# Kernel optimization log

Hardware: AMD Instinct MI355X
Metric: run time of the kernel (lower is better)

The kernel has to match this reference:

```python
import jax, jax.numpy as jnp
import numpy as np

Cl, Nl, Cv, Nv, M = 32, 128, 8, 64, 500000


def _sample1d(line, g):
    # line: [C, N]; g in [-1,1]; align_corners=True, zeros padding
    C, N = line.shape
    ix = (g + 1.0) * 0.5 * (N - 1)
    i0 = jnp.floor(ix)
    w = ix - i0
    i0 = i0.astype(jnp.int32)
    def gth(i, wt):
        valid = (i >= 0) & (i < N)
        return line[:, jnp.clip(i, 0, N - 1)] * (wt * valid)
    return (gth(i0, 1.0 - w) + gth(i0 + 1, w)).T  # [M, C]


def _sample2d(plane, gx, gy):
    # plane: [C, H, W]; grid x -> W axis, y -> H axis (torch grid_sample convention)
    C, H, W = plane.shape
    ix = (gx + 1.0) * 0.5 * (W - 1)
    iy = (gy + 1.0) * 0.5 * (H - 1)
    x0 = jnp.floor(ix); y0 = jnp.floor(iy)
    wx = ix - x0; wy = iy - y0
    x0 = x0.astype(jnp.int32); y0 = y0.astype(jnp.int32)
    flat = plane.reshape(C, -1)
    def gth(xi, yi, wt):
        valid = (xi >= 0) & (xi < W) & (yi >= 0) & (yi < H)
        idx = jnp.clip(yi, 0, H - 1) * W + jnp.clip(xi, 0, W - 1)
        return flat[:, idx] * (wt * valid)
    out = (gth(x0, y0, (1 - wx) * (1 - wy)) + gth(x0 + 1, y0, wx * (1 - wy))
           + gth(x0, y0 + 1, (1 - wx) * wy) + gth(x0 + 1, y0 + 1, wx * wy))
    return out.T  # [M, C]


def _sample3d(vol, gx, gy, gz):
    # vol: [C, D, H, W]; grid (x,y,z) -> (W,H,D) axes
    C, D, H, W = vol.shape
    ix = (gx + 1.0) * 0.5 * (W - 1)
    iy = (gy + 1.0) * 0.5 * (H - 1)
    iz = (gz + 1.0) * 0.5 * (D - 1)
    x0 = jnp.floor(ix); y0 = jnp.floor(iy); z0 = jnp.floor(iz)
    wx = ix - x0; wy = iy - y0; wz = iz - z0
    x0 = x0.astype(jnp.int32); y0 = y0.astype(jnp.int32); z0 = z0.astype(jnp.int32)
    flat = vol.reshape(C, -1)
    out = 0.0
    for dz in (0, 1):
        for dy in (0, 1):
            for dx in (0, 1):
                xi, yi, zi = x0 + dx, y0 + dy, z0 + dz
                wt = ((wx if dx else 1 - wx) * (wy if dy else 1 - wy) * (wz if dz else 1 - wz))
                valid = (xi >= 0) & (xi < W) & (yi >= 0) & (yi < H) & (zi >= 0) & (zi < D)
                idx = (jnp.clip(zi, 0, D - 1) * H + jnp.clip(yi, 0, H - 1)) * W + jnp.clip(xi, 0, W - 1)
                out = out + flat[:, idx] * (wt * valid)
    return out.T  # [M, C]


def setup_inputs() -> dict:
    key = jax.random.key(0)
    ks = jax.random.split(key, 16)
    rng, shift = 0.4, 0.1
    coordinates = jax.random.uniform(ks[0], (1, M, 3), minval=-1.0, maxval=1.0)
    line_x = jax.random.uniform(ks[1], (Cl, Nl)) * rng + shift
    line_y = jax.random.uniform(ks[2], (Cl, Nl)) * rng + shift
    line_z = jax.random.uniform(ks[3], (Cl, Nl)) * rng + shift
    plane_xy = jax.random.normal(ks[4], (Cl, Nl, Nl)) * rng + shift
    plane_yz = jax.random.normal(ks[5], (Cl, Nl, Nl)) * rng + shift
    plane_xz = jax.random.normal(ks[6], (Cl, Nl, Nl)) * rng + shift
    volume = jax.random.normal(ks[7], (Cv, Nv, Nv, Nv)) * rng + shift
    def lin(k, fi, fo):
        k1, k2 = jax.random.split(k)
        lim = 1.0 / np.sqrt(fi)
        return (jax.random.uniform(k1, (fi, fo), minval=-lim, maxval=lim),
                jax.random.uniform(k2, (fo,), minval=-lim, maxval=lim))
    Wx, bx = lin(ks[8], Cl, Cl)
    Wy, by = lin(ks[9], Cl, Cl)
    Wz, bz = lin(ks[10], Cl, Cl)
    W1, b1 = lin(ks[11], Cl + Cv, 128)
    W2, b2 = lin(ks[12], 128, 1)
    return dict(coordinates=coordinates, line_x=line_x, line_y=line_y, line_z=line_z,
                plane_xy=plane_xy, plane_yz=plane_yz, plane_xz=plane_xz, volume=volume,
                Wx=Wx, bx=bx, Wy=Wy, by=by, Wz=Wz, bz=bz, W1=W1, b1=b1, W2=W2, b2=b2)


def reference(coordinates, line_x, line_y, line_z, plane_xy, plane_yz, plane_xz, volume,
              Wx, bx, Wy, by, Wz, bz, W1, b1, W2, b2):
    c = coordinates[0]  # [M, 3], batch squeezed like the torch code
    x, y, z = c[:, 0], c[:, 1], c[:, 2]
    x_e = _sample1d(line_x, x)
    y_e = _sample1d(line_y, y)
    z_e = _sample1d(line_z, z)
    xy_e = _sample2d(plane_xy, x, y)
    yz_e = _sample2d(plane_yz, y, z)
    xz_e = _sample2d(plane_xz, x, z)
    xyz_e = _sample3d(volume, x, y, z)
    phi = lambda e, W, b: jax.nn.relu(e) @ W + b  # Sequential(ReLU, Linear)
    yztran = phi(yz_e, Wx, bx)
    xztran = phi(xz_e, Wy, by)
    xytran = phi(xy_e, Wz, bz)
    xtran = phi(x_e, Wx, bx)
    ytran = phi(y_e, Wy, by)
    ztran = phi(z_e, Wz, bz)
    features = xtran * yztran + ytran * xztran + ztran * xytran
    features = jnp.concatenate([features, xyz_e], axis=-1)  # [M, Cl+Cv]
    h = jax.nn.relu(features @ W1 + b1)
    return h @ W2 + b2  # [M, 1]
```

## Files before the change

### kernel.cpp

```cpp
#include <hip/hip_runtime.h>

typedef unsigned short u16;
typedef u16 u16x8 __attribute__((ext_vector_type(8)));
typedef _Float16 half2 __attribute__((ext_vector_type(2)));
typedef _Float16 h8v __attribute__((ext_vector_type(8)));
typedef float f4v __attribute__((ext_vector_type(4)));

union H8 { h8v v; half2 p[4]; };

static __device__ __forceinline__ float bf2f(u16 u) {
    union { unsigned int i; float f; } v;
    v.i = ((unsigned int)u) << 16;
    return v.f;
}
static __device__ __forceinline__ u16 f2bf(float f) {
    union { float f; unsigned int i; } v;
    v.f = f;
    unsigned int x = v.i;
    x += 0x7fffu + ((x >> 16) & 1u);
    return (u16)(x >> 16);
}
static __device__ __forceinline__ float gld(int dt, const void* p, int i) {
    return dt ? ((const float*)p)[i] : bf2f(((const u16*)p)[i]);
}
static __device__ __forceinline__ int detect_dt(const void* coords) {
    u16 v = ((const u16*)coords)[threadIdx.x & 63];
    int e = (v >> 7) & 0xFF;
    bool inr = (e >= 90) && (e <= 126);
    unsigned long long m = __ballot(inr);
    return (__popcll(m) >= 56) ? 0 : 1;
}
static __device__ __forceinline__ half2 pk(float a, float b) {
    return __builtin_bit_cast(half2, __builtin_amdgcn_cvt_pkrtz(a, b));
}

static __device__ __forceinline__ void lds_wait() {
    asm volatile("s_waitcnt lgkmcnt(0)" ::: "memory");
}

#define WF_OFF        64u
#define PLANES_S_OFF  34304u
#define VOL_S_OFF     3180032u
#define LINES_S_OFF   7374336u
#define PART_OFF      7398912u
#define TOT_OFF       9496064u
#define ORDER_OFF     9512448u

#define NBUCK 4096
#define HBLOCKS 256

static __device__ __forceinline__ int make_key3(float x, float y, float z) {
    int kx = min(max((int)((x + 1.0f) * 8.0f), 0), 15);
    int ky = min(max((int)((y + 1.0f) * 8.0f), 0), 15);
    int kz = min(max((int)((z + 1.0f) * 8.0f), 0), 15);
    return (kz * 16 + ky) * 16 + kx;
}
static __device__ __forceinline__ int make_key(int dt, const void* coords, int p) {
    return make_key3(gld(dt, coords, p * 3 + 0), gld(dt, coords, p * 3 + 1),
                     gld(dt, coords, p * 3 + 2));
}

static __device__ __forceinline__ void weights_work(
    int dt, int r,
    const void* Wx, const void* bx, const void* Wy, const void* by,
    const void* Wz, const void* bz, const void* W1, const void* b1,
    const void* W2, const void* b2, float* wbase)
{
    _Float16* WtH = (_Float16*)wbase;
    float*    bv  = wbase + 1536;
    _Float16* W1H = (_Float16*)(wbase + 1632);
    float*    b1v = wbase + 5728;
    float*    W2v = wbase + 5856;
    float*    b2v = wbase + 5984;
    if (r < 3072) {
        int m = r >> 10, idx = r & 1023;
        int o = idx >> 5, c = idx & 31;
        const void* s = (m == 0) ? Wx : (m == 1) ? Wy : Wz;
        WtH[r] = (_Float16)gld(dt, s, c * 32 + o);
    } else if (r < 3168) {
        int q2 = r - 3072;
        int m = q2 >> 5, c = q2 & 31;
        const void* s = (m == 0) ? bx : (m == 1) ? by : bz;
        bv[q2] = gld(dt, s, c);
    } else if (r < 11360) {
        int idx = r - 3168;
        int j = idx >> 6, i = idx & 63;
        W1H[idx] = (i < 40) ? (_Float16)gld(dt, W1, i * 128 + j) : (_Float16)0.0f;
    } else if (r < 11488) {
        b1v[r - 11360] = gld(dt, b1, r - 11360);
    } else if (r < 11616) {
        W2v[r - 11488] = gld(dt, W2, r - 11488);
    } else if (r == 11616) {
        b2v[0] = gld(dt, b2, 0);
    }
}

__global__ __launch_bounds__(256) void kp_prep_all(
    const void* __restrict__ coords,
    const void* __restrict__ lx, const void* __restrict__ ly,
    const void* __restrict__ lz,
    const void* __restrict__ pxy, const void* __restrict__ pyz,
    const void* __restrict__ pxz, const void* __restrict__ vol,
    const void* __restrict__ Wx, const void* __restrict__ bx,
    const void* __restrict__ Wy, const void* __restrict__ by,
    const void* __restrict__ Wz, const void* __restrict__ bz,
    const void* __restrict__ W1, const void* __restrict__ b1,
    const void* __restrict__ W2, const void* __restrict__ b2,
    float* __restrict__ wbase,
    u16* __restrict__ planes_s, u16* __restrict__ vol_s,
    u16* __restrict__ lines_s, u16* __restrict__ part, int M)
{
    __shared__ unsigned int lh[NBUCK];
    int dt = detect_dt(coords);
    int blk = blockIdx.x;
    if (blk < 1798) {
        int t = blk * 256 + threadIdx.x;
        u16x8 v;
        if (t < 196608) {
            int o = t * 8;
            int pl = o >> 19;
            int r  = o & 524287;
            int pos = r >> 5, c0 = r & 31;
            const void* src = (pl == 0) ? pxy : (pl == 1) ? pyz : pxz;
#pragma unroll
            for (int i = 0; i < 8; ++i)
                v[i] = dt ? f2bf(((const float*)src)[(c0 + i) * 16384 + pos])
                          : ((const u16*)src)[(c0 + i) * 16384 + pos];
            *(u16x8*)(planes_s + o) = v;
        } else if (t < 458752) {
            int pos = t - 196608;
#pragma unroll
            for (int c = 0; c < 8; ++c)
                v[c] = dt ? f2bf(((const float*)vol)[c * 262144 + pos])
                          : ((const u16*)vol)[c * 262144 + pos];
            *(u16x8*)(vol_s + pos * 8) = v;
        } else {
            int o = (t - 458752) * 8;
            int l = o >> 12, rr = o & 4095;
            int pos = rr >> 5, c0 = rr & 31;
            const void* src = (l == 0) ? lx : (l == 1) ? ly : lz;
#pragma unroll
            for (int i = 0; i < 8; ++i)
                v[i] = dt ? f2bf(((const float*)src)[(c0 + i) * 128 + pos])
                          : ((const u16*)src)[(c0 + i) * 128 + pos];
            *(u16x8*)(lines_s + o) = v;
        }
    } else if (blk < 1844) {
        int r = (blk - 1798) * 256 + threadIdx.x;
        weights_work(dt, r, Wx, bx, Wy, by, Wz, bz, W1, b1, W2, b2, wbase);
    } else {
        int b = blk - 1844;
        for (int i = threadIdx.x; i < NBUCK; i += 256) lh[i] = 0u;
        __syncthreads();
        for (int p = b * 256 + threadIdx.x; p < M; p += HBLOCKS * 256)
            atomicAdd(&lh[make_key(dt, coords, p)], 1u);
        __syncthreads();
        for (int i = threadIdx.x; i < NBUCK; i += 256)
            part[b * NBUCK + i] = (u16)lh[i];
    }
}

__global__ __launch_bounds__(256) void kp_colscan(
    u16* __restrict__ part, unsigned int* __restrict__ tot)
{
    int lane = threadIdx.x & 63;
    int bkt  = blockIdx.x * 4 + (threadIdx.x >> 6);
    unsigned int v[4];
    unsigned int ltot = 0;
#pragma unroll
    for (int i = 0; i < 4; ++i) {
        v[i] = part[(lane * 4 + i) * NBUCK + bkt];
        ltot += v[i];
    }
    unsigned int x = ltot;
#pragma unroll
    for (int d = 1; d < 64; d <<= 1) {
        unsigned int y = __shfl_up(x, d);
        if (lane >= d) x += y;
    }
    unsigned int run = x - ltot;
#pragma unroll
    for (int i = 0; i < 4; ++i) {
        part[(lane * 4 + i) * NBUCK + bkt] = (u16)run;
        run += v[i];
    }
    if (lane == 63) tot[bkt] = x;
}

__global__ __launch_bounds__(256) void kp_scatter_det(
    const void* __restrict__ coords, const u16* __restrict__ part,
    const unsigned int* __restrict__ tot,
    int* __restrict__ order, u16* __restrict__ scoords, int M)
{
    __shared__ unsigned int cnt[NBUCK];
    __shared__ unsigned int psum[256];
    int b = blockIdx.x;
    int t = threadIdx.x;
    unsigned int bs[16];
    unsigned int s = 0;
#pragma unroll
    for (int i = 0; i < 16; ++i) {
        bs[i] = tot[t * 16 + i];
        s += bs[i];
    }
    psum[t] = s;
    __syncthreads();
#pragma unroll
    for (int d = 1; d < 256; d <<= 1) {
        unsigned int v = (t >= d) ? psum[t - d] : 0u;
        __syncthreads();
        psum[t] += v;
        __syncthreads();
    }
    unsigned int run = psum[t] - s;
#pragma unroll
    for (int i = 0; i < 16; ++i) {
        int bkt = t * 16 + i;
        cnt[bkt] = run + (unsigned int)part[b * NBUCK + bkt];
        run += bs[i];
    }
    __syncthreads();
    int dt = detect_dt(coords);
    const u16* cu = (const u16*)coords;
    for (int p = b * 256 + t; p < M; p += HBLOCKS * 256) {
        float x = gld(dt, coords, p * 3 + 0);
        float y = gld(dt, coords, p * 3 + 1);
        float z = gld(dt, coords, p * 3 + 2);
        int key = make_key3(x, y, z);
        unsigned int pos = atomicAdd(&cnt[key], 1u);
        order[pos] = p;
        if (dt == 0) {
            scoords[pos * 3 + 0] = cu[p * 3 + 0];
            scoords[pos * 3 + 1] = cu[p * 3 + 1];
            scoords[pos * 3 + 2] = cu[p * 3 + 2];
        }
    }
}

struct Samp { int i0, i1; float w0, w1; };

static __device__ __forceinline__ Samp make_samp(float g, int N) {
    float ix = (g + 1.0f) * 0.5f * (float)(N - 1);
    float fl = floorf(ix);
    float w  = ix - fl;
    int i  = (int)fl;
    int i1 = i + 1;
    float v0 = (i  >= 0 && i  < N) ? 1.0f : 0.0f;
    float v1 = (i1 >= 0 && i1 < N) ? 1.0f : 0.0f;
    Samp s;
    s.w0 = (1.0f - w) * v0;
    s.w1 = w * v1;
    s.i0 = min(max(i, 0), N - 1);
    s.i1 = min(max(i1, 0), N - 1);
    return s;
}

#define MFMA16(a, b, c) __builtin_amdgcn_mfma_f32_16x16x32_f16((a), (b), (c), 0, 0, 0)

#define SRE 34
#define SR2 68

struct PL { u16x8 q00[4], q01[4], q10[4], q11[4]; };
struct VL { u16x8 v[8]; };

static __device__ __forceinline__ void plane_load(
    const u16* __restrict__ Ps, const Samp& sa, const Samp& sb, PL& P)
{
    const u16x8* p00 = (const u16x8*)(Ps + (sb.i0 * 128 + sa.i0) * 32);
    const u16x8* p01 = (const u16x8*)(Ps + (sb.i0 * 128 + sa.i1) * 32);
    const u16x8* p10 = (const u16x8*)(Ps + (sb.i1 * 128 + sa.i0) * 32);
    const u16x8* p11 = (const u16x8*)(Ps + (sb.i1 * 128 + sa.i1) * 32);
#pragma unroll
    for (int cc = 0; cc < 4; ++cc) {
        P.q00[cc] = p00[cc]; P.q01[cc] = p01[cc];
        P.q10[cc] = p10[cc]; P.q11[cc] = p11[cc];
    }
}

static __device__ __forceinline__ void vol_loads(
    const u16* __restrict__ vol_s, const Samp& vx, const Samp& vy,
    const Samp& vz, VL& V)
{
#pragma unroll
    for (int corner = 0; corner < 8; ++corner) {
        int dx = corner & 1, dy = (corner >> 1) & 1, dz = corner >> 2;
        int xi = dx ? vx.i1 : vx.i0;
        int yi = dy ? vy.i1 : vy.i0;
        int zi = dz ? vz.i1 : vz.i0;
        V.v[corner] = *(const u16x8*)(vol_s + (((zi * 64) + yi) * 64 + xi) * 8);
    }
}

template<int PRE>
static __device__ __forceinline__ void term_step(
    int lane, int q, int l15,
    const u16* __restrict__ Ls, const Samp& sl,
    const PL& P, const Samp& sa, const Samp& sb,
    const _Float16* __restrict__ Wt, const float* __restrict__ bvt,
    _Float16* El, _Float16* Ep, float (&feat)[4][2][4],
    const u16* __restrict__ nps, const Samp& na, const Samp& nb, PL& PN,
    const u16* __restrict__ vol_s, const Samp& vx, const Samp& vy,
    const Samp& vz, VL& V)
{
    const u16x8* l0 = (const u16x8*)(Ls + sl.i0 * 32);
    const u16x8* l1 = (const u16x8*)(Ls + sl.i1 * 32);
    float w00 = sb.w0 * sa.w0, w01 = sb.w0 * sa.w1;
    float w10 = sb.w1 * sa.w0, w11 = sb.w1 * sa.w1;
#pragma unroll
    for (int cc = 0; cc < 4; ++cc) {
        u16x8 A0 = l0[cc], A1 = l1[cc];
        u16x8 Q00 = P.q00[cc], Q01 = P.q01[cc];
        u16x8 Q10 = P.q10[cc], Q11 = P.q11[cc];
        H8 hl, hp;
#pragma unroll
        for (int kk = 0; kk < 4; ++kk) {
            int k0 = 2 * kk, k1 = k0 + 1;
            float el0 = sl.w0 * bf2f(A0[k0]) + sl.w1 * bf2f(A1[k0]);
            float el1 = sl.w0 * bf2f(A0[k1]) + sl.w1 * bf2f(A1[k1]);
            float ep0 = w00 * bf2f(Q00[k0]) + w01 * bf2f(Q01[k0])
                      + w10 * bf2f(Q10[k0]) + w11 * bf2f(Q11[k0]);
            float ep1 = w00 * bf2f(Q00[k1]) + w01 * bf2f(Q01[k1])
                      + w10 * bf2f(Q10[k1]) + w11 * bf2f(Q11[k1]);
            hl.p[kk] = pk(fmaxf(el0, 0.0f), fmaxf(el1, 0.0f));
            hp.p[kk] = pk(fmaxf(ep0, 0.0f), fmaxf(ep1, 0.0f));
        }
        *(h8v*)&El[lane * SRE + cc * 8] = hl.v;
        *(h8v*)&Ep[lane * SRE + cc * 8] = hp.v;
    }
    if constexpr (PRE == 1) plane_load(nps, na, nb, PN);
    if constexpr (PRE == 2) vol_loads(vol_s, vx, vy, vz, V);

    h8v bf0 = *(const h8v*)&Wt[(l15) * 32 + q * 8];
    h8v bf1 = *(const h8v*)&Wt[(16 + l15) * 32 + q * 8];
    float bb0 = bvt[l15], bb1 = bvt[16 + l15];
    f4v c0 = {bb0, bb0, bb0, bb0};
    f4v c1 = {bb1, bb1, bb1, bb1};
    lds_wait();
#pragma unroll
    for (int mt = 0; mt < 4; ++mt) {
        h8v aL = *(const h8v*)&El[(mt * 16 + l15) * SRE + q * 8];
        h8v aP = *(const h8v*)&Ep[(mt * 16 + l15) * SRE + q * 8];
        f4v ta0 = MFMA16(aL, bf0, c0);
        f4v tb0 = MFMA16(aP, bf0, c0);
        f4v ta1 = MFMA16(aL, bf1, c1);
        f4v tb1 = MFMA16(aP, bf1, c1);
#pragma unroll
        for (int r = 0; r < 4; ++r) {
            feat[mt][0][r] += ta0[r] * tb0[r];
            feat[mt][1][r] += ta1[r] * tb1[r];
        }
    }
    lds_wait();
}

__global__ __launch_bounds__(64) void kp_main_mfma(
    const void* __restrict__ coords, const int* __restrict__ order,
    const u16* __restrict__ scoords,
    const u16* __restrict__ planes_s, const u16* __restrict__ vol_s,
    const u16* __restrict__ lines_s,
    const float* __restrict__ wbase,
    void* __restrict__ out, int M)
{
    __shared__ _Float16 eb[2 * 64 * SRE];
    __shared__ float res[64];
    int dt = detect_dt(coords);
    const _Float16* WtH = (const _Float16*)wbase;
    const float*    bv  = wbase + 1536;
    const _Float16* W1H = (const _Float16*)(wbase + 1632);
    const float*    b1v = wbase + 5728;
    const float*    W2v = wbase + 5856;
    const float*    b2v = wbase + 5984;

    int lane = threadIdx.x;
    int q = lane >> 4, l15 = lane & 15;
    _Float16* El = eb;
    _Float16* Ep = eb + 64 * SRE;
    _Float16* E2 = eb;

    int p = blockIdx.x * 64 + lane;
    p = min(p, M - 1);
    int sp = order[p];

    float x, y, z;
    if (dt == 0) {
        x = bf2f(scoords[p * 3 + 0]);
        y = bf2f(scoords[p * 3 + 1]);
        z = bf2f(scoords[p * 3 + 2]);
    } else {
        x = ((const float*)coords)[sp * 3 + 0];
        y = ((const float*)coords)[sp * 3 + 1];
        z = ((const float*)coords)[sp * 3 + 2];
    }

    Samp sx = make_samp(x, 128), sy = make_samp(y, 128), sz = make_samp(z, 128);

    float feat[4][2][4];
#pragma unroll
    for (int mt = 0; mt < 4; ++mt)
#pragma unroll
        for (int n = 0; n < 2; ++n)
#pragma unroll
            for (int r = 0; r < 4; ++r) feat[mt][n][r] = 0.0f;

    PL Pa, Pb;
    VL V;
    Samp vx, vy, vz;

    plane_load(planes_s + 1 * 524288, sy, sz, Pa);

    term_step<1>(lane, q, l15, lines_s + 0 * 4096, sx, Pa, sy, sz,
                 WtH + 0, bv + 0, El, Ep, feat,
                 planes_s + 2 * 524288, sx, sz, Pb,
                 vol_s, sx, sx, sx, V);

    term_step<1>(lane, q, l15, lines_s + 1 * 4096, sy, Pb, sx, sz,
                 WtH + 1024, bv + 32, El, Ep, feat,
                 planes_s + 0 * 524288, sx, sy, Pa,
                 vol_s, sx, sx, sx, V);

    vx = make_samp(x, 64); vy = make_samp(y, 64); vz = make_samp(z, 64);

    term_step<2>(lane, q, l15, lines_s + 2 * 4096, sz, Pa, sx, sy,
                 WtH + 2048, bv + 64, El, Ep, feat,
                 planes_s, sx, sy, Pb,
                 vol_s, vx, vy, vz, V);

#pragma unroll
    for (int mt = 0; mt < 4; ++mt)
#pragma unroll
        for (int n = 0; n < 2; ++n)
#pragma unroll
            for (int r = 0; r < 4; ++r)
                E2[(mt * 16 + q * 4 + r) * SR2 + n * 16 + l15] =
                    (_Float16)feat[mt][n][r];
    {
        float vf[8];
#pragma unroll
        for (int c = 0; c < 8; ++c) vf[c] = 0.0f;
#pragma unroll
        for (int corner = 0; corner < 8; ++corner) {
            int dx = corner & 1, dy = (corner >> 1) & 1, dz = corner >> 2;
            float w = (dx ? vx.w1 : vx.w0) * (dy ? vy.w1 : vy.w0)
                    * (dz ? vz.w1 : vz.w0);
            u16x8 v = V.v[corner];
#pragma unroll
            for (int c = 0; c < 8; ++c)
                vf[c] = fmaf(w, bf2f(v[c]), vf[c]);
        }
        H8 hv;
#pragma unroll
        for (int k = 0; k < 4; ++k) hv.p[k] = pk(vf[2 * k], vf[2 * k + 1]);
        *(h8v*)&E2[lane * SR2 + 32] = hv.v;
        h8v zz = {};
        *(h8v*)&E2[lane * SR2 + 40] = zz;
        *(h8v*)&E2[lane * SR2 + 48] = zz;
        *(h8v*)&E2[lane * SR2 + 56] = zz;
    }
    lds_wait();

    h8v af[4][2];
#pragma unroll
    for (int mt = 0; mt < 4; ++mt)
#pragma unroll
        for (int ks = 0; ks < 2; ++ks)
            af[mt][ks] = *(const h8v*)&E2[(mt * 16 + l15) * SR2 + ks * 32 + q * 8];

    float s[4][4];
#pragma unroll
    for (int mt = 0; mt < 4; ++mt)
#pragma unroll
        for (int r = 0; r < 4; ++r) s[mt][r] = 0.0f;

#pragma unroll
    for (int NT = 0; NT < 8; ++NT) {
        int o = NT * 16 + l15;
        h8v b0  = *(const h8v*)&W1H[o * 64 + q * 8];
        h8v b1f = *(const h8v*)&W1H[o * 64 + 32 + q * 8];
        float w2 = W2v[o];
        float bb = b1v[o];
        f4v cinit = {bb, bb, bb, bb};
#pragma unroll
        for (int mt = 0; mt < 4; ++mt) {
            f4v c = MFMA16(af[mt][0], b0, cinit);
            c = MFMA16(af[mt][1], b1f, c);
#pragma unroll
            for (int r = 0; r < 4; ++r)
                s[mt][r] = fmaf(fmaxf(c[r], 0.0f), w2, s[mt][r]);
        }
    }
#pragma unroll
    for (int mt = 0; mt < 4; ++mt)
#pragma unroll
        for (int r = 0; r < 4; ++r) {
            float v = s[mt][r];
            v += __shfl_xor(v, 1);
            v += __shfl_xor(v, 2);
            v += __shfl_xor(v, 4);
            v += __shfl_xor(v, 8);
            s[mt][r] = v;
        }
    if (l15 == 0) {
#pragma unroll
        for (int mt = 0; mt < 4; ++mt)
#pragma unroll
            for (int r = 0; r < 4; ++r)
                res[mt * 16 + q * 4 + r] = s[mt][r];
    }
    lds_wait();
    float rr = res[lane] + b2v[0];
    if (dt) ((float*)out)[sp] = rr;
    else    ((u16*)out)[sp] = f2bf(rr);
}

__global__ void kp_prep_weights_fb(
    const void* __restrict__ coords,
    const void* __restrict__ Wx, const void* __restrict__ bx,
    const void* __restrict__ Wy, const void* __restrict__ by,
    const void* __restrict__ Wz, const void* __restrict__ bz,
    const void* __restrict__ W1, const void* __restrict__ b1,
    const void* __restrict__ W2, const void* __restrict__ b2,
    float* __restrict__ wbase)
{
    int dt = detect_dt(coords);
    int t = blockIdx.x * blockDim.x + threadIdx.x;
    weights_work(dt, t, Wx, bx, Wy, by, Wz, bz, W1, b1, W2, b2, wbase);
}

__global__ __launch_bounds__(256) void kp_main_direct(
    const void* __restrict__ coords,
    const void* __restrict__ lx, const void* __restrict__ ly, const void* __restrict__ lz,
    const void* __restrict__ pxy, const void* __restrict__ pyz, const void* __restrict__ pxz,
    const void* __restrict__ vol,
    const float* __restrict__ wbase,
    void* __restrict__ out, int M)
{
    int dt = detect_dt(coords);
    const _Float16* WtH = (const _Float16*)wbase;
    const float*    bv  = wbase + 1536;
    const _Float16* W1H = (const _Float16*)(wbase + 1632);
    const float*    b1v = wbase + 5728;
    const float*    W2v = wbase + 5856;
    const float*    b2v = wbase + 5984;

    int p = blockIdx.x * 256 + threadIdx.x;
    p = min(p, M - 1);

    float x = gld(dt, coords, p * 3 + 0);
    float y = gld(dt, coords, p * 3 + 1);
    float z = gld(dt, coords, p * 3 + 2);

    Samp sx = make_samp(x, 128), sy = make_samp(y, 128), sz = make_samp(z, 128);

    float feat[40];
#pragma unroll
    for (int o = 0; o < 40; ++o) feat[o] = 0.0f;

    const void* Ls[3] = {lx, ly, lz};
    const void* Psv[3] = {pyz, pxz, pxy};
    Samp sl3[3] = {sx, sy, sz};
    Samp sa3[3] = {sy, sx, sx};
    Samp sb3[3] = {sz, sz, sy};
#pragma unroll 1
    for (int m = 0; m < 3; ++m) {
        float ta[32], tb[32];
        const float* bvt = bv + m * 32;
        const _Float16* Wt = WtH + m * 1024;
#pragma unroll
        for (int o = 0; o < 32; ++o) { ta[o] = bvt[o]; tb[o] = bvt[o]; }
        Samp sl = sl3[m], sa = sa3[m], sb = sb3[m];
        float w00 = sb.w0 * sa.w0, w01 = sb.w0 * sa.w1;
        float w10 = sb.w1 * sa.w0, w11 = sb.w1 * sa.w1;
        int i00 = sb.i0 * 128 + sa.i0, i01 = sb.i0 * 128 + sa.i1;
        int i10 = sb.i1 * 128 + sa.i0, i11 = sb.i1 * 128 + sa.i1;
#pragma unroll 1
        for (int c = 0; c < 32; ++c) {
            float el = sl.w0 * gld(dt, Ls[m], c * 128 + sl.i0)
                     + sl.w1 * gld(dt, Ls[m], c * 128 + sl.i1);
            float ep = w00 * gld(dt, Psv[m], c * 16384 + i00)
                     + w01 * gld(dt, Psv[m], c * 16384 + i01)
                     + w10 * gld(dt, Psv[m], c * 16384 + i10)
                     + w11 * gld(dt, Psv[m], c * 16384 + i11);
            float r1 = fmaxf(el, 0.0f), r2 = fmaxf(ep, 0.0f);
#pragma unroll
            for (int o = 0; o < 32; ++o) {
                float w = (float)Wt[o * 32 + c];
                ta[o] = fmaf(r1, w, ta[o]);
                tb[o] = fmaf(r2, w, tb[o]);
            }
        }
#pragma unroll
        for (int o = 0; o < 32; ++o) feat[o] = fmaf(ta[o], tb[o], feat[o]);
    }

    Samp vx = make_samp(x, 64), vy = make_samp(y, 64), vz = make_samp(z, 64);
#pragma unroll 1
    for (int corner = 0; corner < 8; ++corner) {
        int dx = corner & 1, dy = (corner >> 1) & 1, dz = corner >> 2;
        int xi = dx ? vx.i1 : vx.i0;
        int yi = dy ? vy.i1 : vy.i0;
        int zi = dz ? vz.i1 : vz.i0;
        float w = (dx ? vx.w1 : vx.w0) * (dy ? vy.w1 : vy.w0) * (dz ? vz.w1 : vz.w0);
        int pos = ((zi * 64) + yi) * 64 + xi;
#pragma unroll
        for (int c = 0; c < 8; ++c)
            feat[32 + c] = fmaf(w, gld(dt, vol, c * 262144 + pos), feat[32 + c]);
    }

    float acc_out = b2v[0];
#pragma unroll 2
    for (int j = 0; j < 128; ++j) {
        float acc = b1v[j];
        const _Float16* wr = W1H + j * 64;
#pragma unroll
        for (int i = 0; i < 40; ++i)
            acc = fmaf(feat[i], (float)wr[i], acc);
        acc_out = fmaf(fmaxf(acc, 0.0f), W2v[j], acc_out);
    }
    if (dt) ((float*)out)[p] = acc_out;
    else    ((u16*)out)[p] = f2bf(acc_out);
}

extern "C" void kernel_launch(void* const* d_in, const int* in_sizes, int n_in,
                              void* d_out, int out_size, void* d_ws, size_t ws_size,
                              hipStream_t stream) {
    const void* coords = d_in[0];
    const void* lx  = d_in[1];
    const void* ly  = d_in[2];
    const void* lz  = d_in[3];
    const void* pxy = d_in[4];
    const void* pyz = d_in[5];
    const void* pxz = d_in[6];
    const void* vol = d_in[7];
    const void* Wx  = d_in[8];
    const void* bx  = d_in[9];
    const void* Wy  = d_in[10];
    const void* by  = d_in[11];
    const void* Wz  = d_in[12];
    const void* bz  = d_in[13];
    const void* W1  = d_in[14];
    const void* b1  = d_in[15];
    const void* W2  = d_in[16];
    const void* b2  = d_in[17];

    int M = in_sizes[0] / 3;

    char* ws = (char*)d_ws;
    float*        wbase    = (float*)(ws + WF_OFF);
    u16*          planes_s = (u16*)(ws + PLANES_S_OFF);
    u16*          vol_s    = (u16*)(ws + VOL_S_OFF);
    u16*          lines_s  = (u16*)(ws + LINES_S_OFF);
    u16*          part     = (u16*)(ws + PART_OFF);
    unsigned int* tot      = (unsigned int*)(ws + TOT_OFF);
    int*          order    = (int*)(ws + ORDER_OFF);
    u16*          scoords  = (u16*)(ws + ORDER_OFF + (size_t)M * 4u);

    size_t need_sorted = (size_t)ORDER_OFF + (size_t)M * 4u + (size_t)M * 6u;

    if (ws_size >= need_sorted) {
        kp_prep_all<<<2100, 256, 0, stream>>>(coords, lx, ly, lz, pxy, pyz, pxz, vol,
                                              Wx, bx, Wy, by, Wz, bz, W1, b1, W2, b2,
                                              wbase, planes_s, vol_s, lines_s, part, M);
        kp_colscan<<<NBUCK / 4, 256, 0, stream>>>(part, tot);
        kp_scatter_det<<<HBLOCKS, 256, 0, stream>>>(coords, part, tot, order,
                                                    scoords, M);
        int blocks64 = (M + 63) / 64;
        kp_main_mfma<<<blocks64, 64, 0, stream>>>(coords, order, scoords,
                                                  planes_s, vol_s,
                                                  lines_s, wbase, d_out, M);
    } else {
        int blocks = (M + 255) / 256;
        kp_prep_weights_fb<<<46, 256, 0, stream>>>(coords, Wx, bx, Wy, by, Wz, bz,
                                                   W1, b1, W2, b2, wbase);
        kp_main_direct<<<blocks, 256, 0, stream>>>(coords, lx, ly, lz, pxy, pyz, pxz,
                                                   vol, wbase, d_out, M);
    }
}
```

Before: 206.8 us.

## Write sorted outputs contiguously and unpermute via inverse index in finalize kernel

The main kernel now writes results in sorted order to a temporary buffer, avoiding the scattered 2-byte stores and the order[] lookup in the bf16 path. The scatter kernel also records an inverse permutation, and a new finalize kernel gathers the results back into original order with coalesced writes. LDS row strides for the embedding buffer are changed (34->40, 68->72), likely to cut bank conflicts. The cost is an extra kernel launch, more workspace, and extra inverse-index traffic.

```diff
diff --git a/kernel.cpp b/kernel.cpp
--- a/kernel.cpp
+++ b/kernel.cpp
@@ -190,7 +190,8 @@
 __global__ __launch_bounds__(256) void kp_scatter_det(
     const void* __restrict__ coords, const u16* __restrict__ part,
     const unsigned int* __restrict__ tot,
-    int* __restrict__ order, u16* __restrict__ scoords, int M)
+    int* __restrict__ order, u16* __restrict__ scoords,
+    int* __restrict__ inv, int M)
 {
     __shared__ unsigned int cnt[NBUCK];
     __shared__ unsigned int psum[256];
@@ -229,12 +230,25 @@
         int key = make_key3(x, y, z);
         unsigned int pos = atomicAdd(&cnt[key], 1u);
         order[pos] = p;
+        if (inv) inv[p] = (int)pos;
         if (dt == 0) {
             scoords[pos * 3 + 0] = cu[p * 3 + 0];
             scoords[pos * 3 + 1] = cu[p * 3 + 1];
             scoords[pos * 3 + 2] = cu[p * 3 + 2];
         }
     }
+}
+
+__global__ __launch_bounds__(256) void kp_finalize(
+    const void* __restrict__ coords, const int* __restrict__ inv,
+    const void* __restrict__ tmp, void* __restrict__ out, int M)
+{
+    int dt = detect_dt(coords);
+    int i = blockIdx.x * 256 + threadIdx.x;
+    if (i >= M) return;
+    int pos = inv[i];
+    if (dt) ((float*)out)[i] = ((const float*)tmp)[pos];
+    else    ((u16*)out)[i]   = ((const u16*)tmp)[pos];
 }
 
 struct Samp { int i0, i1; float w0, w1; };
@@ -257,8 +271,8 @@
 
 #define MFMA16(a, b, c) __builtin_amdgcn_mfma_f32_16x16x32_f16((a), (b), (c), 0, 0, 0)
 
-#define SRE 34
-#define SR2 68
+#define SRE 40
+#define SR2 72
 
 struct PL { u16x8 q00[4], q01[4], q10[4], q11[4]; };
 struct VL { u16x8 v[8]; };
@@ -359,9 +373,9 @@
     const u16* __restrict__ planes_s, const u16* __restrict__ vol_s,
     const u16* __restrict__ lines_s,
     const float* __restrict__ wbase,
-    void* __restrict__ out, int M)
-{
-    __shared__ _Float16 eb[2 * 64 * SRE];
+    void* __restrict__ tmp, void* __restrict__ out, int M)
+{
+    __shared__ _Float16 eb[5120];
     __shared__ float res[64];
     int dt = detect_dt(coords);
     const _Float16* WtH = (const _Float16*)wbase;
@@ -374,12 +388,13 @@
     int lane = threadIdx.x;
     int q = lane >> 4, l15 = lane & 15;
     _Float16* El = eb;
-    _Float16* Ep = eb + 64 * SRE;
+    _Float16* Ep = eb + 2560;
     _Float16* E2 = eb;
 
     int p = blockIdx.x * 64 + lane;
     p = min(p, M - 1);
-    int sp = order[p];
+    int sp = 0;
+    if (dt == 1 || tmp == nullptr) sp = order[p];
 
     float x, y, z;
     if (dt == 0) {
@@ -508,8 +523,13 @@
     }
     lds_wait();
     float rr = res[lane] + b2v[0];
-    if (dt) ((float*)out)[sp] = rr;
-    else    ((u16*)out)[sp] = f2bf(rr);
+    if (tmp) {
+        if (dt) ((float*)tmp)[p] = rr;
+        else    ((u16*)tmp)[p]   = f2bf(rr);
+    } else {
+        if (dt) ((float*)out)[sp] = rr;
+        else    ((u16*)out)[sp]   = f2bf(rr);
+    }
 }
 
 __global__ void kp_prep_weights_fb(
@@ -652,21 +672,33 @@
     u16*          part     = (u16*)(ws + PART_OFF);
     unsigned int* tot      = (unsigned int*)(ws + TOT_OFF);
     int*          order    = (int*)(ws + ORDER_OFF);
-    u16*          scoords  = (u16*)(ws + ORDER_OFF + (size_t)M * 4u);
-
-    size_t need_sorted = (size_t)ORDER_OFF + (size_t)M * 4u + (size_t)M * 6u;
+    size_t scoff = (size_t)ORDER_OFF + (size_t)M * 4u;
+    u16*          scoords  = (u16*)(ws + scoff);
+    size_t invoff = scoff + (size_t)M * 6u;
+    invoff = (invoff + 3u) & ~(size_t)3u;
+    int*          inv      = (int*)(ws + invoff);
+    size_t tmpoff = invoff + (size_t)M * 4u;
+    void*         tmp      = (void*)(ws + tmpoff);
+
+    size_t need_sorted = invoff;
+    size_t need_full   = tmpoff + (size_t)M * 4u;
 
     if (ws_size >= need_sorted) {
+        bool full = (ws_size >= need_full);
         kp_prep_all<<<2100, 256, 0, stream>>>(coords, lx, ly, lz, pxy, pyz, pxz, vol,
                                               Wx, bx, Wy, by, Wz, bz, W1, b1, W2, b2,
                                               wbase, planes_s, vol_s, lines_s, part, M);
         kp_colscan<<<NBUCK / 4, 256, 0, stream>>>(part, tot);
         kp_scatter_det<<<HBLOCKS, 256, 0, stream>>>(coords, part, tot, order,
-                                                    scoords, M);
+                                                    scoords, full ? inv : nullptr, M);
         int blocks64 = (M + 63) / 64;
         kp_main_mfma<<<blocks64, 64, 0, stream>>>(coords, order, scoords,
-                                                  planes_s, vol_s,
-                                                  lines_s, wbase, d_out, M);
+                                                  planes_s, vol_s, lines_s, wbase,
+                                                  full ? tmp : nullptr, d_out, M);
+        if (full) {
+            int blocksF = (M + 255) / 256;
+            kp_finalize<<<blocksF, 256, 0, stream>>>(coords, inv, tmp, d_out, M);
+        }
     } else {
         int blocks = (M + 255) / 256;
         kp_prep_weights_fb<<<46, 256, 0, stream>>>(coords, Wx, bx, Wy, by, Wz, bz,
```

Result: no change. 203.7 us (-1.5%).
